# Kernel optimization log

Hardware: AMD Instinct MI355X
Metric: run time of the kernel (lower is better)

Reference implementation:

```python
import jax, jax.numpy as jnp
import numpy as np

# Human3.6M-style 17-joint skeleton: joint 0 is the root (pelvis)
PARENTS = np.array([-1, 0, 1, 2, 0, 4, 5, 0, 7, 8, 9, 8, 11, 12, 8, 14, 15])
NUM_JOINTS = 17
NUM_BONES = 16
# Unit T-pose direction operator per joint (row 0 = root, unused)
T_POSE_OPERATORS = np.array([
    [0., 0., 0.],    # 0 pelvis (root)
    [-1., 0., 0.],   # 1 right hip
    [0., -1., 0.],   # 2 right knee
    [0., -1., 0.],   # 3 right ankle
    [1., 0., 0.],    # 4 left hip
    [0., -1., 0.],   # 5 left knee
    [0., -1., 0.],   # 6 left ankle
    [0., 1., 0.],    # 7 spine
    [0., 1., 0.],    # 8 thorax
    [0., 1., 0.],    # 9 neck
    [0., 1., 0.],    # 10 head
    [1., 0., 0.],    # 11 left shoulder
    [1., 0., 0.],    # 12 left elbow
    [1., 0., 0.],    # 13 left wrist
    [-1., 0., 0.],   # 14 right shoulder
    [-1., 0., 0.],   # 15 right elbow
    [-1., 0., 0.],   # 16 right wrist
], dtype=np.float32)

EPS = 1e-8


def _normalize(v):
    return v / jnp.maximum(jnp.linalg.norm(v, axis=-1, keepdims=True), EPS)


def rot6d_to_matrix(r6):
    """Zhou et al. ortho6d -> rotation matrix. r6: [N, 6] -> [N, 3, 3]."""
    x_raw, y_raw = r6[:, 0:3], r6[:, 3:6]
    x = _normalize(x_raw)
    z = _normalize(jnp.cross(x, y_raw))
    y = jnp.cross(z, x)
    # columns of R are x, y, z
    return jnp.stack([x, y, z], axis=-1)  # [N, 3, 3]


def pose_decoder_forward(rotations_repr, bones_lengths_repr, root_positions):
    BL, J, _ = rotations_repr.shape
    B = bones_lengths_repr.shape[0]
    L = BL // B
    # replicate bone lengths over frames: [B, nb] -> [BL, nb, 1]
    bones_length = jnp.broadcast_to(
        bones_lengths_repr[:, None, :], (B, L, NUM_BONES)
    ).reshape(BL, NUM_BONES, 1)

    # rotation matrices [BL, J, 3, 3]
    R = rot6d_to_matrix(rotations_repr.reshape(-1, 6)).reshape(BL, J, 3, 3)

    # T-pose from bone lengths (17-step tree accumulation)
    ops = jnp.asarray(T_POSE_OPERATORS)
    offsets = ops[1:][None, :, :] * bones_length  # [BL, nb, 3]
    t_pose = [jnp.zeros((BL, 3), dtype=rotations_repr.dtype)]
    for j in range(1, NUM_JOINTS):
        t_pose.append(t_pose[PARENTS[j]] + offsets[:, j - 1])

    # forward kinematics: sequential gather+rotate+accumulate over the tree
    positions_world = [root_positions]
    rotations_world = [R[:, 0]]
    for j in range(1, NUM_JOINTS):
        p = int(PARENTS[j])
        off = t_pose[j] - t_pose[p]  # [BL, 3]
        pos = jnp.einsum('bij,bj->bi', rotations_world[p], off) + positions_world[p]
        positions_world.append(pos)
        rotations_world.append(jnp.einsum('bij,bjk->bik', rotations_world[p], R[:, j]))
    return jnp.stack(positions_world, axis=1)  # [BL, 17, 3]


def setup_inputs() -> dict:
    key = jax.random.key(0)
    k1, k2, k3 = jax.random.split(key, 3)
    BL, B = 131072, 512
    rotations_repr = jax.random.normal(k1, (BL, NUM_JOINTS, 6), dtype=jnp.float32)
    bones_lengths_repr = jax.random.uniform(k2, (B, NUM_BONES), dtype=jnp.float32)
    root_positions = jax.random.normal(k3, (BL, 3), dtype=jnp.float32)
    return {
        'rotations_repr': rotations_repr,
        'bones_lengths_repr': bones_lengths_repr,
        'root_positions': root_positions,
    }


def reference(rotations_repr, bones_lengths_repr, root_positions):
    return pose_decoder_forward(rotations_repr, bones_lengths_repr, root_positions)
```

## Files before the change

kernel.cpp:

```cpp
#include <hip/hip_runtime.h>

#define TPB 64
#define NFLT 102

typedef const __attribute__((address_space(1))) void g_void;
typedef __attribute__((address_space(3))) void lds_void;

struct M3 { float a[9]; };
struct V3 { float x, y, z; };

__device__ __forceinline__ void fence_lgkm() {
    asm volatile("s_waitcnt lgkmcnt(0)" ::: "memory");
    __builtin_amdgcn_wave_barrier();
}

__device__ __forceinline__ M3 rot6d2(const float2* v) {
    float x0 = v[0].x, x1 = v[0].y, x2 = v[1].x;
    float y0 = v[1].y, y1 = v[2].x, y2 = v[2].y;
    float inx = rsqrtf(fmaxf(x0*x0 + x1*x1 + x2*x2, 1e-16f));
    x0 *= inx; x1 *= inx; x2 *= inx;
    float z0 = x1*y2 - x2*y1;
    float z1 = x2*y0 - x0*y2;
    float z2 = x0*y1 - x1*y0;
    float inz = rsqrtf(fmaxf(z0*z0 + z1*z1 + z2*z2, 1e-16f));
    z0 *= inz; z1 *= inz; z2 *= inz;
    float w0 = z1*x2 - z2*x1;
    float w1 = z2*x0 - z0*x2;
    float w2 = z0*x1 - z1*x0;
    M3 R;
    R.a[0] = x0; R.a[1] = w0; R.a[2] = z0;
    R.a[3] = x1; R.a[4] = w1; R.a[5] = z1;
    R.a[6] = x2; R.a[7] = w2; R.a[8] = z2;
    return R;
}

__device__ __forceinline__ M3 m3mul(const M3& A, const M3& B) {
    M3 C;
#pragma unroll
    for (int r = 0; r < 3; ++r)
#pragma unroll
        for (int c = 0; c < 3; ++c)
            C.a[3*r + c] = A.a[3*r + 0] * B.a[0 + c]
                         + A.a[3*r + 1] * B.a[3 + c]
                         + A.a[3*r + 2] * B.a[6 + c];
    return C;
}

__device__ __forceinline__ V3 step(const M3& P, V3 pp, int axis, float s) {
    V3 q;
    q.x = pp.x + s * P.a[0 + axis];
    q.y = pp.y + s * P.a[3 + axis];
    q.z = pp.z + s * P.a[6 + axis];
    return q;
}

__device__ __forceinline__ void put(float* so, int j, V3 q) {
    so[3*j + 0] = q.x; so[3*j + 1] = q.y; so[3*j + 2] = q.z;
}

__device__ __forceinline__ void fk_from_regs(const float2* v, float* so,
                                             const float* len,
                                             float rx, float ry, float rz) {
    V3 q0; q0.x = rx; q0.y = ry; q0.z = rz;
    so[0] = rx; so[1] = ry; so[2] = rz;
    M3 W0 = rot6d2(v + 0);

    M3 W1 = m3mul(W0, rot6d2(v + 3*1));  V3 q1 = step(W0, q0, 0, -len[0]);  put(so, 1, q1);
    M3 W2 = m3mul(W1, rot6d2(v + 3*2));  V3 q2 = step(W1, q1, 1, -len[1]);  put(so, 2, q2);
                             V3 q3 = step(W2, q2, 1, -len[2]);  put(so, 3, q3);

    M3 W4 = m3mul(W0, rot6d2(v + 3*4));  V3 q4 = step(W0, q0, 0,  len[3]);  put(so, 4, q4);
    M3 W5 = m3mul(W4, rot6d2(v + 3*5));  V3 q5 = step(W4, q4, 1, -len[4]);  put(so, 5, q5);
                             V3 q6 = step(W5, q5, 1, -len[5]);  put(so, 6, q6);

    M3 W7 = m3mul(W0, rot6d2(v + 3*7));  V3 q7 = step(W0, q0, 1,  len[6]);  put(so, 7, q7);
    M3 W8 = m3mul(W7, rot6d2(v + 3*8));  V3 q8 = step(W7, q7, 1,  len[7]);  put(so, 8, q8);

    M3 W9 = m3mul(W8, rot6d2(v + 3*9));  V3 q9 = step(W8, q8, 1,  len[8]);  put(so, 9, q9);
                            V3 q10 = step(W9, q9, 1, len[9]);  put(so, 10, q10);

    M3 W11 = m3mul(W8,  rot6d2(v + 3*11)); V3 q11 = step(W8,  q8,  0, len[10]); put(so, 11, q11);
    M3 W12 = m3mul(W11, rot6d2(v + 3*12)); V3 q12 = step(W11, q11, 0, len[11]); put(so, 12, q12);
                              V3 q13 = step(W12, q12, 0, len[12]); put(so, 13, q13);

    M3 W14 = m3mul(W8,  rot6d2(v + 3*14)); V3 q14 = step(W8,  q8,  0, -len[13]); put(so, 14, q14);
    M3 W15 = m3mul(W14, rot6d2(v + 3*15)); V3 q15 = step(W14, q14, 0, -len[14]); put(so, 15, q15);
                              V3 q16 = step(W15, q15, 0, -len[15]); put(so, 16, q16);
}

__global__ __launch_bounds__(TPB) void PoseDecoder_kernel(
    const float* __restrict__ rot,
    const float* __restrict__ bones,
    const float* __restrict__ root,
    float* __restrict__ out,
    int BL, int L)
{
    __shared__ __align__(16) float s_buf[TPB * NFLT];
    const int t = threadIdx.x;
    const long long base = (long long)blockIdx.x * TPB;

    const bool full = (base + TPB <= BL) &&
                      (base / L == (base + TPB - 1) / L);

    if (full) {
        const char* gb = (const char*)rot + (size_t)base * 408;
#pragma unroll
        for (int r = 0; r < 25; ++r)
            __builtin_amdgcn_global_load_lds(
                (g_void*)(gb + r * 1024 + t * 16),
                (lds_void*)((char*)s_buf + r * 1024), 16, 0, 0);
        __builtin_amdgcn_global_load_lds((g_void*)(gb + 25600 + t * 4),
                (lds_void*)((char*)s_buf + 25600), 4, 0, 0);
        __builtin_amdgcn_global_load_lds((g_void*)(gb + 25856 + t * 4),
                (lds_void*)((char*)s_buf + 25856), 4, 0, 0);

        const long long gs = base + t;
        float rx = root[gs*3 + 0], ry = root[gs*3 + 1], rz = root[gs*3 + 2];
        const float* bl = bones + (size_t)(base / L) * 16;
        float len[16];
#pragma unroll
        for (int k = 0; k < 16; ++k) len[k] = bl[k];

        asm volatile("s_waitcnt vmcnt(0) lgkmcnt(0)" ::: "memory");
        __builtin_amdgcn_wave_barrier();

        float2 v[51];
        const float2* l2 = (const float2*)((const char*)s_buf + t * 408);
#pragma unroll
        for (int k = 0; k < 51; ++k) v[k] = l2[k];
        fence_lgkm();

        fk_from_regs(v, s_buf + t * 51, len, rx, ry, rz);
        fence_lgkm();

        float4* o4 = (float4*)(out + (size_t)base * 51);
        const float4* l4 = (const float4*)s_buf;
#pragma unroll
        for (int r = 0; r < 12; ++r) o4[r * 64 + t] = l4[r * 64 + t];
        if (t < 48) o4[768 + t] = l4[768 + t];
    } else {
        const int nv = (int)((BL - base) < TPB ? (BL - base) : TPB);
        for (int e = t; e < nv * NFLT; e += TPB)
            s_buf[e] = rot[(size_t)base * NFLT + e];
        const long long gs = base + (t < nv ? t : 0);
        float rx = root[gs*3 + 0], ry = root[gs*3 + 1], rz = root[gs*3 + 2];
        const float* bl = bones + (size_t)(gs / L) * 16;
        float len[16];
#pragma unroll
        for (int k = 0; k < 16; ++k) len[k] = bl[k];
        asm volatile("s_waitcnt vmcnt(0) lgkmcnt(0)" ::: "memory");
        __builtin_amdgcn_wave_barrier();

        float2 v[51];
        const float2* l2 = (const float2*)((const char*)s_buf + t * 408);
#pragma unroll
        for (int k = 0; k < 51; ++k) v[k] = (t < nv) ? l2[k] : make_float2(0.f, 0.f);
        fence_lgkm();
        if (t < nv) fk_from_regs(v, s_buf + t * 51, len, rx, ry, rz);
        fence_lgkm();
        for (int e = t; e < nv * 51; e += TPB)
            out[(size_t)base * 51 + e] = s_buf[e];
    }
}

extern "C" void kernel_launch(void* const* d_in, const int* in_sizes, int n_in,
                              void* d_out, int out_size, void* d_ws, size_t ws_size,
                              hipStream_t stream) {
    const float* rot   = (const float*)d_in[0];
    const float* bones = (const float*)d_in[1];
    const float* root  = (const float*)d_in[2];
    float* out = (float*)d_out;

    int BL = in_sizes[0] / 102;
    int B  = in_sizes[1] / 16;
    int L  = BL / B;

    int grid = (BL + TPB - 1) / TPB;
    PoseDecoder_kernel<<<grid, TPB, 0, stream>>>(rot, bones, root, out, BL, L);
}
```

Before: 20.76 us.

## Load only used joint rotations directly from global memory, skipping LDS staging

Replaces the coalesced global-to-LDS bulk copy of all 17 joint 6D rotations with direct per-thread float2 global loads of only the 12 joints whose rotations are actually consumed; leaf joints' rotations are never loaded. This cuts read traffic by about 30% and removes the LDS staging buffer, roughly halving shared memory per block. In exchange the per-thread strided loads (408-byte stride) are much less coalesced, which may hurt memory efficiency since 64-byte lines are only partially used per request.

```diff
diff --git a/kernel.cpp b/kernel.cpp
--- a/kernel.cpp
+++ b/kernel.cpp
@@ -1,10 +1,6 @@
 #include <hip/hip_runtime.h>
 
 #define TPB 64
-#define NFLT 102
-
-typedef const __attribute__((address_space(1))) void g_void;
-typedef __attribute__((address_space(3))) void lds_void;
 
 struct M3 { float a[9]; };
 struct V3 { float x, y, z; };
@@ -58,34 +54,34 @@
     so[3*j + 0] = q.x; so[3*j + 1] = q.y; so[3*j + 2] = q.z;
 }
 
-__device__ __forceinline__ void fk_from_regs(const float2* v, float* so,
+__device__ __forceinline__ void fk_from_regs(const float2 v[12][3], float* so,
                                              const float* len,
                                              float rx, float ry, float rz) {
     V3 q0; q0.x = rx; q0.y = ry; q0.z = rz;
     so[0] = rx; so[1] = ry; so[2] = rz;
-    M3 W0 = rot6d2(v + 0);
+    M3 W0 = rot6d2(v[0]);
 
-    M3 W1 = m3mul(W0, rot6d2(v + 3*1));  V3 q1 = step(W0, q0, 0, -len[0]);  put(so, 1, q1);
-    M3 W2 = m3mul(W1, rot6d2(v + 3*2));  V3 q2 = step(W1, q1, 1, -len[1]);  put(so, 2, q2);
-                             V3 q3 = step(W2, q2, 1, -len[2]);  put(so, 3, q3);
+    M3 W1 = m3mul(W0, rot6d2(v[1]));  V3 q1 = step(W0, q0, 0, -len[0]);  put(so, 1, q1);
+    M3 W2 = m3mul(W1, rot6d2(v[2]));  V3 q2 = step(W1, q1, 1, -len[1]);  put(so, 2, q2);
+                          V3 q3 = step(W2, q2, 1, -len[2]);  put(so, 3, q3);
 
-    M3 W4 = m3mul(W0, rot6d2(v + 3*4));  V3 q4 = step(W0, q0, 0,  len[3]);  put(so, 4, q4);
-    M3 W5 = m3mul(W4, rot6d2(v + 3*5));  V3 q5 = step(W4, q4, 1, -len[4]);  put(so, 5, q5);
-                             V3 q6 = step(W5, q5, 1, -len[5]);  put(so, 6, q6);
+    M3 W4 = m3mul(W0, rot6d2(v[3]));  V3 q4 = step(W0, q0, 0,  len[3]);  put(so, 4, q4);
+    M3 W5 = m3mul(W4, rot6d2(v[4]));  V3 q5 = step(W4, q4, 1, -len[4]);  put(so, 5, q5);
+                          V3 q6 = step(W5, q5, 1, -len[5]);  put(so, 6, q6);
 
-    M3 W7 = m3mul(W0, rot6d2(v + 3*7));  V3 q7 = step(W0, q0, 1,  len[6]);  put(so, 7, q7);
-    M3 W8 = m3mul(W7, rot6d2(v + 3*8));  V3 q8 = step(W7, q7, 1,  len[7]);  put(so, 8, q8);
+    M3 W7 = m3mul(W0, rot6d2(v[5]));  V3 q7 = step(W0, q0, 1,  len[6]);  put(so, 7, q7);
+    M3 W8 = m3mul(W7, rot6d2(v[6]));  V3 q8 = step(W7, q7, 1,  len[7]);  put(so, 8, q8);
 
-    M3 W9 = m3mul(W8, rot6d2(v + 3*9));  V3 q9 = step(W8, q8, 1,  len[8]);  put(so, 9, q9);
-                            V3 q10 = step(W9, q9, 1, len[9]);  put(so, 10, q10);
+    M3 W9 = m3mul(W8, rot6d2(v[7]));  V3 q9 = step(W8, q8, 1,  len[8]);  put(so, 9, q9);
+                         V3 q10 = step(W9, q9, 1, len[9]);  put(so, 10, q10);
 
-    M3 W11 = m3mul(W8,  rot6d2(v + 3*11)); V3 q11 = step(W8,  q8,  0, len[10]); put(so, 11, q11);
-    M3 W12 = m3mul(W11, rot6d2(v + 3*12)); V3 q12 = step(W11, q11, 0, len[11]); put(so, 12, q12);
-                              V3 q13 = step(W12, q12, 0, len[12]); put(so, 13, q13);
+    M3 W11 = m3mul(W8,  rot6d2(v[8]));  V3 q11 = step(W8,  q8,  0, len[10]); put(so, 11, q11);
+    M3 W12 = m3mul(W11, rot6d2(v[9]));  V3 q12 = step(W11, q11, 0, len[11]); put(so, 12, q12);
+                           V3 q13 = step(W12, q12, 0, len[12]); put(so, 13, q13);
 
-    M3 W14 = m3mul(W8,  rot6d2(v + 3*14)); V3 q14 = step(W8,  q8,  0, -len[13]); put(so, 14, q14);
-    M3 W15 = m3mul(W14, rot6d2(v + 3*15)); V3 q15 = step(W14, q14, 0, -len[14]); put(so, 15, q15);
-                              V3 q16 = step(W15, q15, 0, -len[15]); put(so, 16, q16);
+    M3 W14 = m3mul(W8,  rot6d2(v[10])); V3 q14 = step(W8,  q8,  0, -len[13]); put(so, 14, q14);
+    M3 W15 = m3mul(W14, rot6d2(v[11])); V3 q15 = step(W14, q14, 0, -len[14]); put(so, 15, q15);
+                           V3 q16 = step(W15, q15, 0, -len[15]); put(so, 16, q16);
 }
 
 __global__ __launch_bounds__(TPB) void PoseDecoder_kernel(
@@ -95,71 +91,49 @@
     float* __restrict__ out,
     int BL, int L)
 {
-    __shared__ __align__(16) float s_buf[TPB * NFLT];
+    __shared__ __align__(16) float s_out[TPB * 51];
     const int t = threadIdx.x;
     const long long base = (long long)blockIdx.x * TPB;
+    const long long gs = base + t;
+    const bool ok = gs < BL;
 
-    const bool full = (base + TPB <= BL) &&
-                      (base / L == (base + TPB - 1) / L);
+    constexpr int UJ[12] = {0, 1, 2, 4, 5, 7, 8, 9, 11, 12, 14, 15};
 
-    if (full) {
-        const char* gb = (const char*)rot + (size_t)base * 408;
+    float2 v[12][3];
+    const float2* g2 = (const float2*)(rot + (size_t)(ok ? gs : 0) * 102);
 #pragma unroll
-        for (int r = 0; r < 25; ++r)
-            __builtin_amdgcn_global_load_lds(
-                (g_void*)(gb + r * 1024 + t * 16),
-                (lds_void*)((char*)s_buf + r * 1024), 16, 0, 0);
-        __builtin_amdgcn_global_load_lds((g_void*)(gb + 25600 + t * 4),
-                (lds_void*)((char*)s_buf + 25600), 4, 0, 0);
-        __builtin_amdgcn_global_load_lds((g_void*)(gb + 25856 + t * 4),
-                (lds_void*)((char*)s_buf + 25856), 4, 0, 0);
+    for (int u = 0; u < 12; ++u)
+#pragma unroll
+        for (int k = 0; k < 3; ++k)
+            v[u][k] = g2[UJ[u] * 3 + k];
 
-        const long long gs = base + t;
-        float rx = root[gs*3 + 0], ry = root[gs*3 + 1], rz = root[gs*3 + 2];
+    const long long rbase = (ok ? gs : 0) * 3;
+    float rx = root[rbase + 0], ry = root[rbase + 1], rz = root[rbase + 2];
+
+    float len[16];
+    if (base / L == (base + TPB - 1) / L) {
         const float* bl = bones + (size_t)(base / L) * 16;
-        float len[16];
 #pragma unroll
         for (int k = 0; k < 16; ++k) len[k] = bl[k];
+    } else {
+        const float* bl = bones + (size_t)((ok ? gs : 0) / L) * 16;
+#pragma unroll
+        for (int k = 0; k < 16; ++k) len[k] = bl[k];
+    }
 
-        asm volatile("s_waitcnt vmcnt(0) lgkmcnt(0)" ::: "memory");
-        __builtin_amdgcn_wave_barrier();
+    if (ok) fk_from_regs(v, s_out + t * 51, len, rx, ry, rz);
+    fence_lgkm();
 
-        float2 v[51];
-        const float2* l2 = (const float2*)((const char*)s_buf + t * 408);
-#pragma unroll
-        for (int k = 0; k < 51; ++k) v[k] = l2[k];
-        fence_lgkm();
-
-        fk_from_regs(v, s_buf + t * 51, len, rx, ry, rz);
-        fence_lgkm();
-
+    if (base + TPB <= BL) {
         float4* o4 = (float4*)(out + (size_t)base * 51);
-        const float4* l4 = (const float4*)s_buf;
+        const float4* l4 = (const float4*)s_out;
 #pragma unroll
         for (int r = 0; r < 12; ++r) o4[r * 64 + t] = l4[r * 64 + t];
         if (t < 48) o4[768 + t] = l4[768 + t];
     } else {
-        const int nv = (int)((BL - base) < TPB ? (BL - base) : TPB);
-        for (int e = t; e < nv * NFLT; e += TPB)
-            s_buf[e] = rot[(size_t)base * NFLT + e];
-        const long long gs = base + (t < nv ? t : 0);
-        float rx = root[gs*3 + 0], ry = root[gs*3 + 1], rz = root[gs*3 + 2];
-        const float* bl = bones + (size_t)(gs / L) * 16;
-        float len[16];
-#pragma unroll
-        for (int k = 0; k < 16; ++k) len[k] = bl[k];
-        asm volatile("s_waitcnt vmcnt(0) lgkmcnt(0)" ::: "memory");
-        __builtin_amdgcn_wave_barrier();
-
-        float2 v[51];
-        const float2* l2 = (const float2*)((const char*)s_buf + t * 408);
-#pragma unroll
-        for (int k = 0; k < 51; ++k) v[k] = (t < nv) ? l2[k] : make_float2(0.f, 0.f);
-        fence_lgkm();
-        if (t < nv) fk_from_regs(v, s_buf + t * 51, len, rx, ry, rz);
-        fence_lgkm();
-        for (int e = t; e < nv * 51; e += TPB)
-            out[(size_t)base * 51 + e] = s_buf[e];
+        const int nf = (int)(BL - base) * 51;
+        for (int e = t; e < nf; e += TPB)
+            out[(size_t)base * 51 + e] = s_out[e];
     }
 }
 
```

Result: faster. 18.46 us (-11.1%).
